# Performance work log

Hardware: AMD Instinct MI355X
Metric: run time of the kernel (lower is better)

The kernel has to match this reference:

```python
import jax, jax.numpy as jnp
import numpy as np

B, T, E, H = 1, 2048, 2048, 32
D = E // H  # head_dim = 64


def alibi_bias(n_heads, t_q, t_k, dtype):
    # slopes: 2^(-8*(h+1)/n_heads) for power-of-two head counts
    slopes = jnp.power(2.0, -8.0 * jnp.arange(1, n_heads + 1, dtype=jnp.float32) / n_heads)
    i = jnp.arange(t_q)[:, None] + (t_k - t_q)  # absolute query positions
    j = jnp.arange(t_k)[None, :]
    rel = (j - i).astype(dtype)                 # [t_q, t_k], <=0 on/below diagonal
    return (slopes[:, None, None] * rel).astype(dtype)  # [H, t_q, t_k]


def setup_inputs() -> dict:
    key = jax.random.key(0)
    kx, kq, kk, kv, ko = jax.random.split(key, 5)
    s = E ** -0.5
    x = jax.random.normal(kx, (B, T, E), dtype=jnp.float32)
    Wq = jax.random.normal(kq, (E, E), dtype=jnp.float32) * s
    Wk = jax.random.normal(kk, (D, E), dtype=jnp.float32) * s
    Wv = jax.random.normal(kv, (D, E), dtype=jnp.float32) * s
    Wo = jax.random.normal(ko, (E, E), dtype=jnp.float32) * s
    # causal mask: True where attention is disallowed (j > i)
    attention_mask = jnp.triu(jnp.ones((T, T), dtype=bool), k=1)[None, None]  # [1,1,T,T]
    return {"x": x, "Wq": Wq, "Wk": Wk, "Wv": Wv, "Wo": Wo, "attention_mask": attention_mask}


def reference(x, Wq, Wk, Wv, Wo, attention_mask):
    b, t, _ = x.shape
    scale = D ** -0.5
    q = (x @ Wq.T).reshape(b, t, H, D).transpose(0, 2, 1, 3)  # [b,H,t,D]
    k = x @ Wk.T                                              # [b,t,D] (single KV head)
    v = x @ Wv.T                                              # [b,t,D]
    attn = jnp.einsum('bhtd,bsd->bhts', q * scale, k)         # [b,H,t,t]
    attn = attn + alibi_bias(H, t, t, attn.dtype)[None]
    attn = jnp.where(attention_mask, jnp.asarray(-10000.0, attn.dtype), attn)
    w = jax.nn.softmax(attn, axis=-1)
    out = jnp.einsum('bhts,bsd->bhtd', w, v)                  # [b,H,t,D]
    out = out.transpose(0, 2, 1, 3).reshape(b, t, E)
    return out @ Wo.T
```

## Files before the change

kernel.cpp:

```cpp
#include <hip/hip_runtime.h>
#include <stdint.h>

typedef __bf16 bf16;
typedef __bf16 bf16x4 __attribute__((ext_vector_type(4)));
typedef __bf16 bf16x8 __attribute__((ext_vector_type(8)));
typedef short short4v __attribute__((ext_vector_type(4)));
typedef float floatx4 __attribute__((ext_vector_type(4)));

#define MFMA32(a, b, c) __builtin_amdgcn_mfma_f32_16x16x32_bf16((a), (b), (c), 0, 0, 0)

__device__ __forceinline__ floatx4 mfma16(bf16x4 a, bf16x4 b, floatx4 c) {
  return __builtin_amdgcn_mfma_f32_16x16x16bf16_1k(
      __builtin_bit_cast(short4v, a), __builtin_bit_cast(short4v, b), c, 0, 0, 0);
}

__device__ __forceinline__ void gload16(const void* g, void* l) {
  __builtin_amdgcn_global_load_lds(
      (const __attribute__((address_space(1))) void*)g,
      (__attribute__((address_space(3))) void*)l, 16, 0, 0);
}

__device__ __forceinline__ bf16x8 load8(const float* p) {
  float4 lo = *(const float4*)p;
  float4 hi = *(const float4*)(p + 4);
  bf16x8 r;
  r[0] = (bf16)lo.x; r[1] = (bf16)lo.y; r[2] = (bf16)lo.z; r[3] = (bf16)lo.w;
  r[4] = (bf16)hi.x; r[5] = (bf16)hi.y; r[6] = (bf16)hi.z; r[7] = (bf16)hi.w;
  return r;
}

__global__ __launch_bounds__(256) void conv3(const float* __restrict__ a, bf16* __restrict__ ab,
                                             const float* __restrict__ b, bf16* __restrict__ bb,
                                             const float* __restrict__ c, bf16* __restrict__ cb) {
  const int i = blockIdx.x * 256 + threadIdx.x;
  const float* src = blockIdx.y == 0 ? a : (blockIdx.y == 1 ? b : c);
  bf16* dst = blockIdx.y == 0 ? ab : (blockIdx.y == 1 ? bb : cb);
  ((bf16x8*)dst)[i] = load8(src + (size_t)i * 8);
}

__global__ __launch_bounds__(256) void pack_kv(const float* __restrict__ Kf,
                                               const float* __restrict__ Vf,
                                               bf16* __restrict__ Kb,
                                               bf16* __restrict__ Vtb) {
  int i = blockIdx.x * 256 + threadIdx.x;
  if (i < 2048 * 64) {
    Kb[i] = (bf16)Kf[i];
    const int t = i >> 6, d = i & 63;
    Vtb[(size_t)d * 2048 + t] = (bf16)Vf[i];
  }
}

template <typename TC>
__global__ __launch_bounds__(256) void gemm_bt_a(const bf16* __restrict__ A,
                                                 const bf16* __restrict__ B,
                                                 TC* __restrict__ C,
                                                 int M, int N, int K) {
  __shared__ __align__(16) bf16 As[2][64 * 32];
  __shared__ __align__(16) bf16 Bs[2][128 * 32];
  const int tid = threadIdx.x;
  const int wave = tid >> 6, lane = tid & 63;
  const int quad = lane >> 4, l16 = lane & 15;
  const int m0 = blockIdx.y * 64, n0 = blockIdx.x * 128;
  const int wm = (wave >> 1) * 32, wn = (wave & 1) * 64;

  floatx4 acc[2][4];
#pragma unroll
  for (int i = 0; i < 2; i++)
#pragma unroll
    for (int j = 0; j < 4; j++) acc[i][j] = (floatx4)0.f;

  const int srow = tid >> 2, scol = (tid & 3) * 8;
  const bf16* Ap = A + (size_t)(m0 + srow) * K + scol;
  const bf16* Bp = B + (size_t)(n0 + srow) * K + scol;

  auto stage = [&](int k0, int buf) {
    gload16(Ap + k0, (char*)As[buf] + tid * 16);
    gload16(Bp + k0, (char*)Bs[buf] + tid * 16);
    gload16(Bp + (size_t)64 * K + k0, (char*)Bs[buf] + 4096 + tid * 16);
  };
  auto compute = [&](int buf) {
    bf16x8 af[2], bfr[4];
#pragma unroll
    for (int mt = 0; mt < 2; mt++)
      af[mt] = *(const bf16x8*)(&As[buf][(wm + mt * 16 + l16) * 32 + quad * 8]);
#pragma unroll
    for (int nt = 0; nt < 4; nt++)
      bfr[nt] = *(const bf16x8*)(&Bs[buf][(wn + nt * 16 + l16) * 32 + quad * 8]);
#pragma unroll
    for (int mt = 0; mt < 2; mt++)
#pragma unroll
      for (int nt = 0; nt < 4; nt++)
        acc[mt][nt] = MFMA32(af[mt], bfr[nt], acc[mt][nt]);
  };

  stage(0, 0);
  for (int k0 = 0; k0 < K; k0 += 64) {
    __syncthreads();
    if (k0 + 32 < K) stage(k0 + 32, 1);
    compute(0);
    __syncthreads();
    if (k0 + 64 < K) stage(k0 + 64, 0);
    compute(1);
  }

#pragma unroll
  for (int mt = 0; mt < 2; mt++) {
#pragma unroll
    for (int nt = 0; nt < 4; nt++) {
      const int col = n0 + wn + nt * 16 + l16;
      const int row = m0 + wm + mt * 16 + quad * 4;
#pragma unroll
      for (int r = 0; r < 4; r++)
        C[(size_t)(row + r) * N + col] = (TC)acc[mt][nt][r];
    }
  }
}

__global__ __launch_bounds__(256) void kv_gemm(const bf16* __restrict__ xb,
                                               const float* __restrict__ Wk,
                                               const float* __restrict__ Wv,
                                               float* __restrict__ Kf,
                                               float* __restrict__ Vf) {
  __shared__ __align__(16) bf16 As[128 * 40];
  __shared__ __align__(16) bf16 Bs[128 * 40];
  const int tid = threadIdx.x;
  const int wave = tid >> 6, lane = tid & 63;
  const int quad = lane >> 4, l16 = lane & 15;
  const int m0 = blockIdx.y * 128;
  const int kbeg = blockIdx.x * 256, kend = kbeg + 256;
  const int wm = (wave >> 1) * 64, wn = (wave & 1) * 64;

  floatx4 acc[4][4];
#pragma unroll
  for (int i = 0; i < 4; i++)
#pragma unroll
    for (int j = 0; j < 4; j++) acc[i][j] = (floatx4)0.f;

  const int sr = tid >> 2, sc = (tid & 3) * 8;

  for (int k0 = kbeg; k0 < kend; k0 += 32) {
    __syncthreads();
#pragma unroll
    for (int rr = 0; rr < 2; rr++) {
      const int row = sr + rr * 64;
      *(bf16x8*)(&As[row * 40 + sc]) =
          *(const bf16x8*)(&xb[(size_t)(m0 + row) * 2048 + k0 + sc]);
      const float* bsrc = (row < 64) ? &Wk[(size_t)row * 2048 + k0 + sc]
                                     : &Wv[(size_t)(row - 64) * 2048 + k0 + sc];
      *(bf16x8*)(&Bs[row * 40 + sc]) = load8(bsrc);
    }
    __syncthreads();

    bf16x8 af[4], bfr[4];
#pragma unroll
    for (int mt = 0; mt < 4; mt++)
      af[mt] = *(const bf16x8*)(&As[(wm + mt * 16 + l16) * 40 + quad * 8]);
#pragma unroll
    for (int nt = 0; nt < 4; nt++)
      bfr[nt] = *(const bf16x8*)(&Bs[(wn + nt * 16 + l16) * 40 + quad * 8]);
#pragma unroll
    for (int mt = 0; mt < 4; mt++)
#pragma unroll
      for (int nt = 0; nt < 4; nt++)
        acc[mt][nt] = MFMA32(af[mt], bfr[nt], acc[mt][nt]);
  }

#pragma unroll
  for (int mt = 0; mt < 4; mt++) {
#pragma unroll
    for (int nt = 0; nt < 4; nt++) {
      const int col = wn + nt * 16 + l16;
      const int row = m0 + wm + mt * 16 + quad * 4;
      float* dst = (col < 64) ? &Kf[(size_t)row * 64 + col]
                              : &Vf[(size_t)row * 64 + (col - 64)];
#pragma unroll
      for (int r = 0; r < 4; r++) atomicAdd(dst + (size_t)r * 64, acc[mt][nt][r]);
    }
  }
}

__global__ __launch_bounds__(256) void attn_kernel(const bf16* __restrict__ Q,
                                                   const bf16* __restrict__ Kb,
                                                   const bf16* __restrict__ Vtb,
                                                   bf16* __restrict__ O) {
  __shared__ __align__(16) bf16 Ks[64 * 72];
  __shared__ __align__(16) bf16 Vt[64 * 72];
  const int tid = threadIdx.x;
  const int wq = tid >> 6, lane = tid & 63;
  const int quad = lane >> 4, l16 = lane & 15;
  const int h = blockIdx.y;
  const int t = 31 - blockIdx.x;
  const float scale2 = 0.125f * 1.44269504f;
  const float slope2 = exp2f(-0.25f * (float)(h + 1)) * 1.44269504f;

  float cq[4];
#pragma unroll
  for (int r = 0; r < 4; r++) cq[r] = slope2 * (float)(quad * 4 + r);
  const float s16 = slope2 * 16.f;

  const int r0 = tid >> 3, c0 = (tid & 7) * 8;

  const int qi = t * 64 + wq * 16 + l16;
  bf16x8 qf[2];
#pragma unroll
  for (int kk = 0; kk < 2; kk++)
    qf[kk] = *(const bf16x8*)(&Q[(size_t)qi * 2048 + h * 64 + kk * 32 + quad * 8]);

  floatx4 oacc[4];
#pragma unroll
  for (int dt = 0; dt < 4; dt++) oacc[dt] = (floatx4)0.f;
  floatx4 lacc = (floatx4)0.f;
  const bf16x4 ones = {(bf16)1.f, (bf16)1.f, (bf16)1.f, (bf16)1.f};

  bf16x8 kreg[2], vreg[2];
  kreg[0] = *(const bf16x8*)(&Kb[(size_t)r0 * 64 + c0]);
  kreg[1] = *(const bf16x8*)(&Kb[(size_t)(r0 + 32) * 64 + c0]);
  vreg[0] = *(const bf16x8*)(&Vtb[(size_t)r0 * 2048 + c0]);
  vreg[1] = *(const bf16x8*)(&Vtb[(size_t)(r0 + 32) * 2048 + c0]);

  for (int kt = 0; kt <= t; kt++) {
    __syncthreads();
    *(bf16x8*)(&Ks[r0 * 72 + c0]) = kreg[0];
    *(bf16x8*)(&Ks[(r0 + 32) * 72 + c0]) = kreg[1];
    *(bf16x8*)(&Vt[r0 * 72 + c0]) = vreg[0];
    *(bf16x8*)(&Vt[(r0 + 32) * 72 + c0]) = vreg[1];
    __syncthreads();
    if (kt < t) {
      const int kn = (kt + 1) * 64;
      kreg[0] = *(const bf16x8*)(&Kb[(size_t)(kn + r0) * 64 + c0]);
      kreg[1] = *(const bf16x8*)(&Kb[(size_t)(kn + r0 + 32) * 64 + c0]);
      vreg[0] = *(const bf16x8*)(&Vtb[(size_t)r0 * 2048 + kn + c0]);
      vreg[1] = *(const bf16x8*)(&Vtb[(size_t)(r0 + 32) * 2048 + kn + c0]);
    }
    const int k0 = kt * 64;

    floatx4 s[4];
#pragma unroll
    for (int mt = 0; mt < 4; mt++) s[mt] = (floatx4)0.f;
#pragma unroll
    for (int kk = 0; kk < 2; kk++) {
#pragma unroll
      for (int mt = 0; mt < 4; mt++) {
        bf16x8 kf = *(const bf16x8*)(&Ks[(mt * 16 + l16) * 72 + kk * 32 + quad * 8]);
        s[mt] = MFMA32(kf, qf[kk], s[mt]);
      }
    }

    const float base0 = slope2 * (float)(k0 - qi);
    bf16x4 pb[4];
    if (kt < t) {
      float base = base0;
#pragma unroll
      for (int mt = 0; mt < 4; mt++) {
        bf16x4 tb;
#pragma unroll
        for (int r = 0; r < 4; r++)
          tb[r] = (bf16)exp2f(__builtin_fmaf(s[mt][r], scale2, base + cq[r]));
        pb[mt] = tb;
        base += s16;
      }
    } else {
      const int qloc = qi - k0;
      float base = base0;
#pragma unroll
      for (int mt = 0; mt < 4; mt++) {
        bf16x4 tb;
#pragma unroll
        for (int r = 0; r < 4; r++) {
          const int moff = mt * 16 + quad * 4 + r;
          const float p = exp2f(__builtin_fmaf(s[mt][r], scale2, base + cq[r]));
          tb[r] = (moff <= qloc) ? (bf16)p : (bf16)0.f;
        }
        pb[mt] = tb;
        base += s16;
      }
    }

#pragma unroll
    for (int mt = 0; mt < 4; mt++) {
      lacc = mfma16(ones, pb[mt], lacc);
#pragma unroll
      for (int dt = 0; dt < 4; dt++) {
        const bf16x4 va = *(const bf16x4*)(&Vt[(dt * 16 + l16) * 72 + mt * 16 + quad * 4]);
        oacc[dt] = mfma16(va, pb[mt], oacc[dt]);
      }
    }
  }

  const float linv = 1.0f / lacc[0];
#pragma unroll
  for (int dt = 0; dt < 4; dt++) {
    bf16x4 ob;
#pragma unroll
    for (int r = 0; r < 4; r++) ob[r] = (bf16)(oacc[dt][r] * linv);
    *(bf16x4*)(&O[(size_t)qi * 2048 + h * 64 + dt * 16 + quad * 4]) = ob;
  }
}

extern "C" void kernel_launch(void* const* d_in, const int* in_sizes, int n_in,
                              void* d_out, int out_size, void* d_ws,
                              size_t ws_size, hipStream_t stream) {
  (void)in_sizes; (void)n_in; (void)out_size; (void)ws_size;
  const float* x = (const float*)d_in[0];
  const float* Wq = (const float*)d_in[1];
  const float* Wk = (const float*)d_in[2];
  const float* Wv = (const float*)d_in[3];
  const float* Wo = (const float*)d_in[4];
  float* out = (float*)d_out;

  const size_t NE = (size_t)2048 * 2048;
  bf16* xb = (bf16*)d_ws;
  bf16* Wqb = xb + NE;
  bf16* Wob = Wqb + NE;
  bf16* Qb = Wob + NE;
  float* Kf = (float*)(Qb + NE);
  float* Vf = Kf + 2048 * 64;
  bf16* Kb = (bf16*)(Vf + 2048 * 64);
  bf16* Vtb = Kb + 2048 * 64;
  bf16* AO = xb;

  hipMemsetAsync(Kf, 0, 2 * 2048 * 64 * sizeof(float), stream);
  conv3<<<dim3(2048, 3), 256, 0, stream>>>(x, xb, Wq, Wqb, Wo, Wob);
  gemm_bt_a<bf16><<<dim3(16, 32), 256, 0, stream>>>(xb, Wqb, Qb, 2048, 2048, 2048);
  kv_gemm<<<dim3(8, 16), 256, 0, stream>>>(xb, Wk, Wv, Kf, Vf);
  pack_kv<<<512, 256, 0, stream>>>(Kf, Vf, Kb, Vtb);
  attn_kernel<<<dim3(32, 32), 256, 0, stream>>>(Qb, Kb, Vtb, AO);
  gemm_bt_a<float><<<dim3(16, 32), 256, 0, stream>>>(AO, Wob, out, 2048, 2048, 2048);
}
```

Before: 276.5 us.

## Pair causal query tiles per block and read K/V directly from global

The attention kernel now launches half as many blocks, and each block processes query tile 31-x and then tile x, so every block does the same total causal work. The shared-memory staging of K and V^T and its two barriers per iteration are removed. Each wave instead loads its K and V fragments straight from global memory, relying on the small single-head K/V staying in cache. This trades LDS traffic and synchronisation for redundant global/L2 loads across the four waves, and halves the grid to 512 blocks, which may lower occupancy and latency hiding.

```diff
diff --git a/kernel.cpp b/kernel.cpp
--- a/kernel.cpp
+++ b/kernel.cpp
@@ -183,13 +183,10 @@
                                                    const bf16* __restrict__ Kb,
                                                    const bf16* __restrict__ Vtb,
                                                    bf16* __restrict__ O) {
-  __shared__ __align__(16) bf16 Ks[64 * 72];
-  __shared__ __align__(16) bf16 Vt[64 * 72];
   const int tid = threadIdx.x;
   const int wq = tid >> 6, lane = tid & 63;
   const int quad = lane >> 4, l16 = lane & 15;
   const int h = blockIdx.y;
-  const int t = 31 - blockIdx.x;
   const float scale2 = 0.125f * 1.44269504f;
   const float slope2 = exp2f(-0.25f * (float)(h + 1)) * 1.44269504f;
 
@@ -197,104 +194,96 @@
 #pragma unroll
   for (int r = 0; r < 4; r++) cq[r] = slope2 * (float)(quad * 4 + r);
   const float s16 = slope2 * 16.f;
-
-  const int r0 = tid >> 3, c0 = (tid & 7) * 8;
-
-  const int qi = t * 64 + wq * 16 + l16;
-  bf16x8 qf[2];
-#pragma unroll
-  for (int kk = 0; kk < 2; kk++)
-    qf[kk] = *(const bf16x8*)(&Q[(size_t)qi * 2048 + h * 64 + kk * 32 + quad * 8]);
-
-  floatx4 oacc[4];
-#pragma unroll
-  for (int dt = 0; dt < 4; dt++) oacc[dt] = (floatx4)0.f;
-  floatx4 lacc = (floatx4)0.f;
   const bf16x4 ones = {(bf16)1.f, (bf16)1.f, (bf16)1.f, (bf16)1.f};
 
-  bf16x8 kreg[2], vreg[2];
-  kreg[0] = *(const bf16x8*)(&Kb[(size_t)r0 * 64 + c0]);
-  kreg[1] = *(const bf16x8*)(&Kb[(size_t)(r0 + 32) * 64 + c0]);
-  vreg[0] = *(const bf16x8*)(&Vtb[(size_t)r0 * 2048 + c0]);
-  vreg[1] = *(const bf16x8*)(&Vtb[(size_t)(r0 + 32) * 2048 + c0]);
-
-  for (int kt = 0; kt <= t; kt++) {
-    __syncthreads();
-    *(bf16x8*)(&Ks[r0 * 72 + c0]) = kreg[0];
-    *(bf16x8*)(&Ks[(r0 + 32) * 72 + c0]) = kreg[1];
-    *(bf16x8*)(&Vt[r0 * 72 + c0]) = vreg[0];
-    *(bf16x8*)(&Vt[(r0 + 32) * 72 + c0]) = vreg[1];
-    __syncthreads();
-    if (kt < t) {
-      const int kn = (kt + 1) * 64;
-      kreg[0] = *(const bf16x8*)(&Kb[(size_t)(kn + r0) * 64 + c0]);
-      kreg[1] = *(const bf16x8*)(&Kb[(size_t)(kn + r0 + 32) * 64 + c0]);
-      vreg[0] = *(const bf16x8*)(&Vtb[(size_t)r0 * 2048 + kn + c0]);
-      vreg[1] = *(const bf16x8*)(&Vtb[(size_t)(r0 + 32) * 2048 + kn + c0]);
-    }
-    const int k0 = kt * 64;
-
-    floatx4 s[4];
-#pragma unroll
-    for (int mt = 0; mt < 4; mt++) s[mt] = (floatx4)0.f;
-#pragma unroll
-    for (int kk = 0; kk < 2; kk++) {
+  auto run_tile = [&](int t) {
+    const int qi = t * 64 + wq * 16 + l16;
+    bf16x8 qf[2];
+#pragma unroll
+    for (int kk = 0; kk < 2; kk++)
+      qf[kk] = *(const bf16x8*)(&Q[(size_t)qi * 2048 + h * 64 + kk * 32 + quad * 8]);
+
+    floatx4 oacc[4];
+#pragma unroll
+    for (int dt = 0; dt < 4; dt++) oacc[dt] = (floatx4)0.f;
+    floatx4 lacc = (floatx4)0.f;
+
+    for (int kt = 0; kt <= t; kt++) {
+      const int k0 = kt * 64;
+
+      floatx4 s[4];
+#pragma unroll
+      for (int mt = 0; mt < 4; mt++) s[mt] = (floatx4)0.f;
+      bf16x8 kf[2][4];
+#pragma unroll
+      for (int kk = 0; kk < 2; kk++)
+#pragma unroll
+        for (int mt = 0; mt < 4; mt++)
+          kf[kk][mt] = *(const bf16x8*)(&Kb[(size_t)(k0 + mt * 16 + l16) * 64 +
+                                            kk * 32 + quad * 8]);
+      bf16x4 va[4][4];
+#pragma unroll
+      for (int dt = 0; dt < 4; dt++)
+#pragma unroll
+        for (int mt = 0; mt < 4; mt++)
+          va[dt][mt] = *(const bf16x4*)(&Vtb[(size_t)(dt * 16 + l16) * 2048 +
+                                             k0 + mt * 16 + quad * 4]);
+#pragma unroll
+      for (int kk = 0; kk < 2; kk++)
+#pragma unroll
+        for (int mt = 0; mt < 4; mt++) s[mt] = MFMA32(kf[kk][mt], qf[kk], s[mt]);
+
+      const float base0 = slope2 * (float)(k0 - qi);
+      bf16x4 pb[4];
+      if (kt < t) {
+        float base = base0;
+#pragma unroll
+        for (int mt = 0; mt < 4; mt++) {
+          bf16x4 tb;
+#pragma unroll
+          for (int r = 0; r < 4; r++)
+            tb[r] = (bf16)exp2f(__builtin_fmaf(s[mt][r], scale2, base + cq[r]));
+          pb[mt] = tb;
+          base += s16;
+        }
+      } else {
+        const int qloc = qi - k0;
+        float base = base0;
+#pragma unroll
+        for (int mt = 0; mt < 4; mt++) {
+          bf16x4 tb;
+#pragma unroll
+          for (int r = 0; r < 4; r++) {
+            const int moff = mt * 16 + quad * 4 + r;
+            const float p = exp2f(__builtin_fmaf(s[mt][r], scale2, base + cq[r]));
+            tb[r] = (moff <= qloc) ? (bf16)p : (bf16)0.f;
+          }
+          pb[mt] = tb;
+          base += s16;
+        }
+      }
+
 #pragma unroll
       for (int mt = 0; mt < 4; mt++) {
-        bf16x8 kf = *(const bf16x8*)(&Ks[(mt * 16 + l16) * 72 + kk * 32 + quad * 8]);
-        s[mt] = MFMA32(kf, qf[kk], s[mt]);
+        lacc = mfma16(ones, pb[mt], lacc);
+#pragma unroll
+        for (int dt = 0; dt < 4; dt++)
+          oacc[dt] = mfma16(va[dt][mt], pb[mt], oacc[dt]);
       }
     }
 
-    const float base0 = slope2 * (float)(k0 - qi);
-    bf16x4 pb[4];
-    if (kt < t) {
-      float base = base0;
-#pragma unroll
-      for (int mt = 0; mt < 4; mt++) {
-        bf16x4 tb;
-#pragma unroll
-        for (int r = 0; r < 4; r++)
-          tb[r] = (bf16)exp2f(__builtin_fmaf(s[mt][r], scale2, base + cq[r]));
-        pb[mt] = tb;
-        base += s16;
-      }
-    } else {
-      const int qloc = qi - k0;
-      float base = base0;
-#pragma unroll
-      for (int mt = 0; mt < 4; mt++) {
-        bf16x4 tb;
-#pragma unroll
-        for (int r = 0; r < 4; r++) {
-          const int moff = mt * 16 + quad * 4 + r;
-          const float p = exp2f(__builtin_fmaf(s[mt][r], scale2, base + cq[r]));
-          tb[r] = (moff <= qloc) ? (bf16)p : (bf16)0.f;
-        }
-        pb[mt] = tb;
-        base += s16;
-      }
-    }
-
-#pragma unroll
-    for (int mt = 0; mt < 4; mt++) {
-      lacc = mfma16(ones, pb[mt], lacc);
-#pragma unroll
-      for (int dt = 0; dt < 4; dt++) {
-        const bf16x4 va = *(const bf16x4*)(&Vt[(dt * 16 + l16) * 72 + mt * 16 + quad * 4]);
-        oacc[dt] = mfma16(va, pb[mt], oacc[dt]);
-      }
-    }
-  }
-
-  const float linv = 1.0f / lacc[0];
-#pragma unroll
-  for (int dt = 0; dt < 4; dt++) {
-    bf16x4 ob;
-#pragma unroll
-    for (int r = 0; r < 4; r++) ob[r] = (bf16)(oacc[dt][r] * linv);
-    *(bf16x4*)(&O[(size_t)qi * 2048 + h * 64 + dt * 16 + quad * 4]) = ob;
-  }
+    const float linv = 1.0f / lacc[0];
+#pragma unroll
+    for (int dt = 0; dt < 4; dt++) {
+      bf16x4 ob;
+#pragma unroll
+      for (int r = 0; r < 4; r++) ob[r] = (bf16)(oacc[dt][r] * linv);
+      *(bf16x4*)(&O[(size_t)qi * 2048 + h * 64 + dt * 16 + quad * 4]) = ob;
+    }
+  };
+
+  run_tile(31 - blockIdx.x);
+  run_tile(blockIdx.x);
 }
 
 extern "C" void kernel_launch(void* const* d_in, const int* in_sizes, int n_in,
@@ -324,6 +313,6 @@
   gemm_bt_a<bf16><<<dim3(16, 32), 256, 0, stream>>>(xb, Wqb, Qb, 2048, 2048, 2048);
   kv_gemm<<<dim3(8, 16), 256, 0, stream>>>(xb, Wk, Wv, Kf, Vf);
   pack_kv<<<512, 256, 0, stream>>>(Kf, Vf, Kb, Vtb);
-  attn_kernel<<<dim3(32, 32), 256, 0, stream>>>(Qb, Kb, Vtb, AO);
+  attn_kernel<<<dim3(16, 32), 256, 0, stream>>>(Qb, Kb, Vtb, AO);
   gemm_bt_a<float><<<dim3(16, 32), 256, 0, stream>>>(AO, Wob, out, 2048, 2048, 2048);
 }
```

Result: slower. 375.8 us (+35.9%).

## Use 128-query attention blocks with double-buffered K/V tiles

Applied to the files above, without the earlier changes.

Each attention block now covers 128 queries with 8 waves (512 threads) instead of 64 queries with 4 waves, so every K/V tile staged in LDS serves twice as many queries. K/V shared tiles are double-buffered, which removes one barrier per iteration. Tiles lying wholly above the causal diagonal for a given wave are skipped. Block order is interleaved across heads to balance the causal triangle. The price is fewer blocks in the grid, and waves idling at the barrier while other waves in the block process the diagonal tiles.

```diff
diff --git a/kernel.cpp b/kernel.cpp
--- a/kernel.cpp
+++ b/kernel.cpp
@@ -179,17 +179,18 @@
   }
 }
 
-__global__ __launch_bounds__(256) void attn_kernel(const bf16* __restrict__ Q,
+__global__ __launch_bounds__(512) void attn_kernel(const bf16* __restrict__ Q,
                                                    const bf16* __restrict__ Kb,
                                                    const bf16* __restrict__ Vtb,
                                                    bf16* __restrict__ O) {
-  __shared__ __align__(16) bf16 Ks[64 * 72];
-  __shared__ __align__(16) bf16 Vt[64 * 72];
+  __shared__ __align__(16) bf16 Ks[2][64 * 72];
+  __shared__ __align__(16) bf16 Vt[2][64 * 72];
   const int tid = threadIdx.x;
-  const int wq = tid >> 6, lane = tid & 63;
+  const int wq = tid >> 6;
+  const int lane = tid & 63;
   const int quad = lane >> 4, l16 = lane & 15;
   const int h = blockIdx.y;
-  const int t = 31 - blockIdx.x;
+  const int t = (blockIdx.y < 16) ? (15 - blockIdx.x) : blockIdx.x;
   const float scale2 = 0.125f * 1.44269504f;
   const float slope2 = exp2f(-0.25f * (float)(h + 1)) * 1.44269504f;
 
@@ -197,10 +198,9 @@
 #pragma unroll
   for (int r = 0; r < 4; r++) cq[r] = slope2 * (float)(quad * 4 + r);
   const float s16 = slope2 * 16.f;
-
-  const int r0 = tid >> 3, c0 = (tid & 7) * 8;
-
-  const int qi = t * 64 + wq * 16 + l16;
+  const bf16x4 ones = {(bf16)1.f, (bf16)1.f, (bf16)1.f, (bf16)1.f};
+
+  const int qi = t * 128 + wq * 16 + l16;
   bf16x8 qf[2];
 #pragma unroll
   for (int kk = 0; kk < 2; kk++)
@@ -210,29 +210,26 @@
 #pragma unroll
   for (int dt = 0; dt < 4; dt++) oacc[dt] = (floatx4)0.f;
   floatx4 lacc = (floatx4)0.f;
-  const bf16x4 ones = {(bf16)1.f, (bf16)1.f, (bf16)1.f, (bf16)1.f};
-
-  bf16x8 kreg[2], vreg[2];
-  kreg[0] = *(const bf16x8*)(&Kb[(size_t)r0 * 64 + c0]);
-  kreg[1] = *(const bf16x8*)(&Kb[(size_t)(r0 + 32) * 64 + c0]);
-  vreg[0] = *(const bf16x8*)(&Vtb[(size_t)r0 * 2048 + c0]);
-  vreg[1] = *(const bf16x8*)(&Vtb[(size_t)(r0 + 32) * 2048 + c0]);
-
-  for (int kt = 0; kt <= t; kt++) {
-    __syncthreads();
-    *(bf16x8*)(&Ks[r0 * 72 + c0]) = kreg[0];
-    *(bf16x8*)(&Ks[(r0 + 32) * 72 + c0]) = kreg[1];
-    *(bf16x8*)(&Vt[r0 * 72 + c0]) = vreg[0];
-    *(bf16x8*)(&Vt[(r0 + 32) * 72 + c0]) = vreg[1];
-    __syncthreads();
-    if (kt < t) {
+
+  const int r0 = tid >> 3, c0 = (tid & 7) * 8;
+  const int ktmax = 2 * t + 1;
+  const int qw0 = t * 128 + wq * 16;
+
+  bf16x8 kreg = *(const bf16x8*)(&Kb[(size_t)r0 * 64 + c0]);
+  bf16x8 vreg = *(const bf16x8*)(&Vtb[(size_t)r0 * 2048 + c0]);
+
+  for (int kt = 0; kt <= ktmax; kt++) {
+    const int buf = kt & 1;
+    *(bf16x8*)(&Ks[buf][r0 * 72 + c0]) = kreg;
+    *(bf16x8*)(&Vt[buf][r0 * 72 + c0]) = vreg;
+    __syncthreads();
+    if (kt < ktmax) {
       const int kn = (kt + 1) * 64;
-      kreg[0] = *(const bf16x8*)(&Kb[(size_t)(kn + r0) * 64 + c0]);
-      kreg[1] = *(const bf16x8*)(&Kb[(size_t)(kn + r0 + 32) * 64 + c0]);
-      vreg[0] = *(const bf16x8*)(&Vtb[(size_t)r0 * 2048 + kn + c0]);
-      vreg[1] = *(const bf16x8*)(&Vtb[(size_t)(r0 + 32) * 2048 + kn + c0]);
+      kreg = *(const bf16x8*)(&Kb[(size_t)(kn + r0) * 64 + c0]);
+      vreg = *(const bf16x8*)(&Vtb[(size_t)r0 * 2048 + kn + c0]);
     }
     const int k0 = kt * 64;
+    if (k0 > qw0 + 15) continue;
 
     floatx4 s[4];
 #pragma unroll
@@ -241,14 +238,14 @@
     for (int kk = 0; kk < 2; kk++) {
 #pragma unroll
       for (int mt = 0; mt < 4; mt++) {
-        bf16x8 kf = *(const bf16x8*)(&Ks[(mt * 16 + l16) * 72 + kk * 32 + quad * 8]);
+        bf16x8 kf = *(const bf16x8*)(&Ks[buf][(mt * 16 + l16) * 72 + kk * 32 + quad * 8]);
         s[mt] = MFMA32(kf, qf[kk], s[mt]);
       }
     }
 
     const float base0 = slope2 * (float)(k0 - qi);
     bf16x4 pb[4];
-    if (kt < t) {
+    if (k0 + 63 <= qw0) {
       float base = base0;
 #pragma unroll
       for (int mt = 0; mt < 4; mt++) {
@@ -281,7 +278,8 @@
       lacc = mfma16(ones, pb[mt], lacc);
 #pragma unroll
       for (int dt = 0; dt < 4; dt++) {
-        const bf16x4 va = *(const bf16x4*)(&Vt[(dt * 16 + l16) * 72 + mt * 16 + quad * 4]);
+        const bf16x4 va =
+            *(const bf16x4*)(&Vt[buf][(dt * 16 + l16) * 72 + mt * 16 + quad * 4]);
         oacc[dt] = mfma16(va, pb[mt], oacc[dt]);
       }
     }
@@ -324,6 +322,6 @@
   gemm_bt_a<bf16><<<dim3(16, 32), 256, 0, stream>>>(xb, Wqb, Qb, 2048, 2048, 2048);
   kv_gemm<<<dim3(8, 16), 256, 0, stream>>>(xb, Wk, Wv, Kf, Vf);
   pack_kv<<<512, 256, 0, stream>>>(Kf, Vf, Kb, Vtb);
-  attn_kernel<<<dim3(32, 32), 256, 0, stream>>>(Qb, Kb, Vtb, AO);
+  attn_kernel<<<dim3(16, 32), 512, 0, stream>>>(Qb, Kb, Vtb, AO);
   gemm_bt_a<float><<<dim3(16, 32), 256, 0, stream>>>(AO, Wob, out, 2048, 2048, 2048);
 }
```

New measurement: 244.3 us. -11.6%, faster.
